# Kernel tuning notes

Measured on AMD Instinct MI355X. Metric: run time of the kernel, lower is better.

## Reference

```python
import jax, jax.numpy as jnp
import numpy as np


def setup_inputs() -> dict:
    key = jax.random.key(0)
    ks = jax.random.split(key, 8)
    B, C, H, W = 16, 256, 64, 64
    E, heads, R = 256, 8, 64
    s = 0.02  # small init scale in lieu of xavier
    return {
        "x": jax.random.normal(ks[0], (B, C, H, W), dtype=jnp.float32),
        "Wqkv": jax.random.normal(ks[1], (3 * E, C), dtype=jnp.float32) * s,
        "bqkv": jnp.zeros((3 * E,), dtype=jnp.float32),
        "Wr": jax.random.normal(ks[2], (2 * R * heads, C), dtype=jnp.float32) * s,
        "br": jnp.zeros((2 * R * heads,), dtype=jnp.float32),
        "Wout": jax.random.normal(ks[3], (C, E), dtype=jnp.float32) * s,
        "bout": jnp.zeros((C,), dtype=jnp.float32),
        "alpha": jax.random.normal(ks[4], (1,), dtype=jnp.float32),
        "num_heads": heads,
        "num_regions": R,
    }


def reference(x, Wqkv, bqkv, Wr, br, Wout, bout, alpha, num_heads, num_regions):
    B, C, H, W = x.shape
    N = H * W
    E = Wqkv.shape[0] // 3
    d = E // num_heads  # head_dim
    xf = x.reshape(B, C, N)  # [B, C, N]

    # qkv 1x1 conv -> [B, 3E, N] -> [B, h, N, 3d] -> q,k,v [B, h, N, d]
    qkv = jnp.einsum("oc,bcn->bon", Wqkv, xf) + bqkv[:, None]
    qkv = qkv.reshape(B, num_heads, 3 * d, N).transpose(0, 1, 3, 2)
    q, k, v = jnp.split(qkv, 3, axis=-1)

    # region projections: 1x1 conv + softmax over the FULL channel axis (2*R*heads)
    r = jnp.einsum("oc,bcn->bon", Wr, xf) + br[:, None]
    r = jax.nn.softmax(r, axis=1)
    r = r.reshape(B, num_heads, 2 * num_regions, N).transpose(0, 1, 3, 2)
    Rq, Rk = jnp.split(r, 2, axis=-1)  # each [B, h, N, R]

    # pool tokens into regions: [B, h, d, R]
    qr = jnp.einsum("bhnd,bhnr->bhdr", q, Rq)
    kr = jnp.einsum("bhnd,bhnr->bhdr", k, Rk)
    vr = jnp.einsum("bhnd,bhnr->bhdr", v, Rk)

    # region-level attention [B, h, Rq, Rk], scaled by sqrt(head_dim)
    logits = jnp.einsum("bhdq,bhdk->bhqk", qr, kr) / jnp.sqrt(jnp.asarray(d, x.dtype))
    attn = jax.nn.softmax(logits, axis=-1)  # dropout is identity at eval

    # values = v_r @ attn^T -> [B, h, d, Rq]; expand back to tokens via Rq^T
    vals = jnp.einsum("bhdk,bhqk->bhdq", vr, attn)
    vals = jnp.einsum("bhdq,bhnq->bhdn", vals, Rq)  # [B, h, d, N]

    vals = vals.reshape(B, E, N)
    out = jnp.einsum("oe,ben->bon", Wout, vals) + bout[:, None]
    out = out.reshape(B, C, H, W)
    return x + alpha * out
```

## Files before the change

kernel.cpp:

```cpp
#include <hip/hip_runtime.h>
#include <cstdint>

typedef unsigned short ushort_t;
typedef __attribute__((ext_vector_type(4))) unsigned short ushort4_t;
typedef __attribute__((ext_vector_type(8))) unsigned short ushort8_t;
typedef __attribute__((ext_vector_type(8))) __bf16 bf16x8;
typedef __attribute__((ext_vector_type(4))) float f32x4;

constexpr int NB = 16;
constexpr int NC = 256;
constexpr int NN = 4096;
constexpr int NP = 1024;
constexpr int NT = 512;
constexpr int NO = 768;

static __device__ __forceinline__ ushort_t f2b(float f) {
  uint32_t u = __builtin_bit_cast(uint32_t, f);
  u += 0x7FFFu + ((u >> 16) & 1u);
  return (ushort_t)(u >> 16);
}
static __device__ __forceinline__ float b2f(ushort_t h) {
  return __builtin_bit_cast(float, (uint32_t)h << 16);
}
static __device__ __forceinline__ f32x4 mfma16(bf16x8 a, bf16x8 b, f32x4 c) {
  return __builtin_amdgcn_mfma_f32_16x16x32_bf16(a, b, c, 0, 0, 0);
}
typedef __attribute__((address_space(1))) const unsigned int guint;
typedef __attribute__((address_space(3))) unsigned int luint;
static __device__ __forceinline__ void glds16(const void* g, void* l) {
  __builtin_amdgcn_global_load_lds((guint*)g, (luint*)l, 16, 0, 0);
}

template <int KITERS>
__device__ __forceinline__ void gemm_core(const ushort_t* __restrict__ Asrc, size_t lda,
                                          const ushort_t* __restrict__ Bsrc, size_t ldb,
                                          ushort_t* SH, f32x4 (&acc)[4][4], int tid) {
  const int l = tid & 63, w = tid >> 6;
  const int fr = l & 15, kq = (l >> 4) * 8;
  const int rr = l >> 3;
  const int sc = ((l & 7) ^ rr) << 3;
  const int swz = (fr & 7) << 3;
  const int wm = (w >> 1) * 64, wn = (w & 1) * 64;

  auto STAGE = [&](int bi, size_t k0) {
    ushort_t* Ad = SH + bi * 8192;
    ushort_t* Bd = SH + 16384 + bi * 8192;
#pragma unroll
    for (int i = 0; i < 4; i++) {
      const int row = i * 32 + w * 8 + rr;
      glds16(Asrc + (size_t)row * lda + k0 + sc, Ad + (i * 32 + w * 8) * 64);
      glds16(Bsrc + (size_t)row * ldb + k0 + sc, Bd + (i * 32 + w * 8) * 64);
    }
  };

  STAGE(0, 0);
  __syncthreads();
  int cur = 0;
#pragma unroll 1
  for (int it = 0; it < KITERS; it++) {
    if (it + 1 < KITERS) STAGE(cur ^ 1, (size_t)(it + 1) * 64);
    const ushort_t* Ar = SH + cur * 8192;
    const ushort_t* Br = SH + 16384 + cur * 8192;
#pragma unroll
    for (int ks = 0; ks < 2; ks++) {
      const int col = ks * 32 + kq;
      bf16x8 af[4], bf[4];
#pragma unroll
      for (int f = 0; f < 4; f++) {
        af[f] = *(const bf16x8*)&Ar[(wm + f * 16 + fr) * 64 + (col ^ swz)];
        bf[f] = *(const bf16x8*)&Br[(wn + f * 16 + fr) * 64 + (col ^ swz)];
      }
#pragma unroll
      for (int fm = 0; fm < 4; fm++)
#pragma unroll
        for (int fn = 0; fn < 4; fn++)
          acc[fm][fn] = mfma16(af[fm], bf[fn], acc[fm][fn]);
    }
    __syncthreads();
    cur ^= 1;
  }
}

__global__ __launch_bounds__(256) void k0_cvt(const float* __restrict__ x,
                                              ushort_t* __restrict__ xb,
                                              ushort_t* __restrict__ xt) {
  __shared__ ushort_t tr[64][88];
  const int tid = threadIdx.x;
  const int n0 = blockIdx.x * 64, c0 = blockIdx.y * 64, b = blockIdx.z;
  const int cr = (tid >> 4) * 4;
  const int nc4 = (tid & 15) * 4;
#pragma unroll
  for (int i = 0; i < 4; i++) {
    size_t idx = ((size_t)b * NC + c0 + cr + i) * NN + n0 + nc4;
    float4 v = *(const float4*)(x + idx);
    ushort4_t o;
    o[0] = f2b(v.x); o[1] = f2b(v.y); o[2] = f2b(v.z); o[3] = f2b(v.w);
    *(ushort4_t*)(xb + idx) = o;
    tr[nc4 + 0][cr + i] = o[0];
    tr[nc4 + 1][cr + i] = o[1];
    tr[nc4 + 2][cr + i] = o[2];
    tr[nc4 + 3][cr + i] = o[3];
  }
  __syncthreads();
  const int nr = tid >> 2, cc0 = (tid & 3) * 16;
  size_t odx = ((size_t)b * NN + n0 + nr) * NC + c0 + cc0;
  *(ushort8_t*)(xt + odx) = *(const ushort8_t*)&tr[nr][cc0];
  *(ushort8_t*)(xt + odx + 8) = *(const ushort8_t*)&tr[nr][cc0 + 8];
}

__global__ __launch_bounds__(256) void cvt_f2b_k(const float* __restrict__ src,
                                                 ushort_t* __restrict__ dst) {
  int i = (blockIdx.x * 256 + threadIdx.x) * 4;
  float4 v = *(const float4*)(src + i);
  ushort4_t o;
  o[0] = f2b(v.x); o[1] = f2b(v.y); o[2] = f2b(v.z); o[3] = f2b(v.w);
  *(ushort4_t*)(dst + i) = o;
}

__global__ __launch_bounds__(256) void k1_proj(const ushort_t* __restrict__ Wrb,
                                               const ushort_t* __restrict__ xt,
                                               const float* __restrict__ br,
                                               ushort_t* __restrict__ P) {
  __shared__ __align__(16) ushort_t SH[4 * 8192];
  const int tid = threadIdx.x;
  const int ord = blockIdx.x;
  const int L = (ord & 7) * 512 + (ord >> 3);
  const int m0 = (L & 7) * 128;
  const int n0 = ((L >> 3) & 31) * 128;
  const int b = L >> 8;
  const int lane = tid & 63, w = tid >> 6;
  const int wm = (w >> 1) * 64, wn = (w & 1) * 64;
  f32x4 acc[4][4] = {};
  gemm_core<4>(Wrb + (size_t)m0 * NC, NC,
               xt + ((size_t)b * NN + n0) * NC, NC, SH, acc, tid);
  const int col = lane & 15, rb = (lane >> 4) * 4;
#pragma unroll
  for (int fm = 0; fm < 4; fm++)
#pragma unroll
    for (int rg = 0; rg < 4; rg++) {
      int row = wm + fm * 16 + rb + rg;
      float bias = br[m0 + row];
#pragma unroll
      for (int fn = 0; fn < 4; fn++)
        SH[row * 136 + wn + fn * 16 + col] = f2b(acc[fm][fn][rg] + bias);
    }
  __syncthreads();
  const int orow = tid >> 1, half = tid & 1;
  const ushort_t* src = &SH[orow * 136 + half * 64];
  ushort_t* dst = P + ((size_t)b * NP + m0 + orow) * NN + n0 + half * 64;
#pragma unroll
  for (int j = 0; j < 8; j++)
    *(ushort8_t*)(dst + j * 8) = *(const ushort8_t*)(src + j * 8);
}

__global__ __launch_bounds__(512) void k2_softmax(ushort_t* __restrict__ P,
                                                  float* __restrict__ sPpart) {
  __shared__ float red[64][64];
  __shared__ float Mf[64], If[64];
  const int tid = threadIdx.x;
  const int n0 = blockIdx.x * 64, b = blockIdx.y;
  const int cg = tid & 7, pg = tid >> 3;
  ushort_t* base = P + (size_t)b * NP * NN + n0 + cg * 8;

  ushort8_t v[16];
  float m[8];
#pragma unroll
  for (int j = 0; j < 8; j++) m[j] = -3.0e38f;
#pragma unroll
  for (int r = 0; r < 16; r++) {
    v[r] = *(const ushort8_t*)(base + (size_t)(pg * 16 + r) * NN);
#pragma unroll
    for (int j = 0; j < 8; j++) m[j] = fmaxf(m[j], b2f(v[r][j]));
  }
#pragma unroll
  for (int j = 0; j < 8; j++) red[pg][cg * 8 + j] = m[j];
  __syncthreads();
  if (tid < 64) {
    float M = -3.0e38f;
    for (int g = 0; g < 64; g++) M = fmaxf(M, red[g][tid]);
    Mf[tid] = M;
  }
  __syncthreads();
  float mj[8], s[8];
#pragma unroll
  for (int j = 0; j < 8; j++) { mj[j] = Mf[cg * 8 + j]; s[j] = 0.f; }
#pragma unroll
  for (int r = 0; r < 16; r++)
#pragma unroll
    for (int j = 0; j < 8; j++) s[j] += __expf(b2f(v[r][j]) - mj[j]);
#pragma unroll
  for (int j = 0; j < 8; j++) red[pg][cg * 8 + j] = s[j];
  __syncthreads();
  if (tid < 64) {
    float S = 0.f;
    for (int g = 0; g < 64; g++) S += red[g][tid];
    If[tid] = 1.f / S;
  }
  __syncthreads();
  float ij[8];
#pragma unroll
  for (int j = 0; j < 8; j++) ij[j] = If[cg * 8 + j];
#pragma unroll
  for (int r = 0; r < 16; r++) {
    int p = pg * 16 + r;
    ushort8_t o;
    float rs = 0.f;
#pragma unroll
    for (int j = 0; j < 8; j++) {
      float e = __expf(b2f(v[r][j]) - mj[j]) * ij[j];
      o[j] = f2b(e);
      rs += e;
    }
    *(ushort8_t*)(base + (size_t)p * NN) = o;
    rs += __shfl_xor(rs, 1, 64);
    rs += __shfl_xor(rs, 2, 64);
    rs += __shfl_xor(rs, 4, 64);
    if (cg == 0) sPpart[((size_t)blockIdx.x * NB + b) * NP + p] = rs;
  }
}

__global__ __launch_bounds__(256) void k2r_reduce(const float* __restrict__ sPpart,
                                                  float* __restrict__ sP) {
  int idx = blockIdx.x * 256 + threadIdx.x;
  float s = 0.f;
#pragma unroll 8
  for (int bx = 0; bx < 64; bx++) s += sPpart[(size_t)bx * (NB * NP) + idx];
  sP[idx] = s;
}

__global__ __launch_bounds__(256) void k3_pool(const ushort_t* __restrict__ xb,
                                               const ushort_t* __restrict__ P,
                                               float* __restrict__ XR4) {
  __shared__ __align__(16) ushort_t SH[4 * 8192];
  const int tid = threadIdx.x;
  const int ord = blockIdx.x;
  const int L = (ord & 7) * 64 + (ord >> 3);
  const int m0 = (L & 1) * 128;
  const int n0 = ((L >> 1) & 7) * 128;
  const int zz = L >> 4;
  const int b = zz >> 1, ks = zz & 1;
  const int lane = tid & 63, w = tid >> 6;
  const int wm = (w >> 1) * 64, wn = (w & 1) * 64;
  f32x4 acc[4][4] = {};
  const size_t kbeg = (size_t)ks * 2048;
  gemm_core<32>(xb + ((size_t)b * NC + m0) * NN + kbeg, NN,
                P + ((size_t)b * NP + n0) * NN + kbeg, NN, SH, acc, tid);
  const int col = lane & 15, rb = (lane >> 4) * 4;
  float* outp = XR4 + (size_t)(ks * NB + b) * NC * NP;
#pragma unroll
  for (int fm = 0; fm < 4; fm++)
#pragma unroll
    for (int fn = 0; fn < 4; fn++)
#pragma unroll
      for (int rg = 0; rg < 4; rg++) {
        int row = m0 + wm + fm * 16 + rb + rg;
        int cc = n0 + wn + fn * 16 + col;
        outp[(size_t)row * NP + cc] = acc[fm][fn][rg];
      }
}

__global__ __launch_bounds__(256) void k3r_tr(const float* __restrict__ XR4,
                                              ushort_t* __restrict__ XRbT) {
  __shared__ ushort_t tr[64][72];
  const int tid = threadIdx.x;
  const int p0 = blockIdx.x * 64, c0 = blockIdx.y * 64, b = blockIdx.z;
  const size_t slice = (size_t)NB * NC * NP;
  const int row = tid >> 4, col4 = (tid & 15) * 4;
#pragma unroll
  for (int i = 0; i < 4; i++) {
    int c = row + i * 16;
    size_t idx = ((size_t)b * NC + c0 + c) * NP + p0 + col4;
    float4 v0 = *(const float4*)(XR4 + idx);
    float4 v1 = *(const float4*)(XR4 + idx + slice);
    tr[col4 + 0][c] = f2b(v0.x + v1.x);
    tr[col4 + 1][c] = f2b(v0.y + v1.y);
    tr[col4 + 2][c] = f2b(v0.z + v1.z);
    tr[col4 + 3][c] = f2b(v0.w + v1.w);
  }
  __syncthreads();
  const int prow = tid >> 2, coff = (tid & 3) * 16;
  size_t odx = ((size_t)b * NP + p0 + prow) * NC + c0 + coff;
  *(ushort8_t*)(XRbT + odx) = *(const ushort8_t*)&tr[prow][coff];
  *(ushort8_t*)(XRbT + odx + 8) = *(const ushort8_t*)&tr[prow][coff + 8];
}

__global__ __launch_bounds__(256) void k4a_qkvr(const ushort_t* __restrict__ Wqkvb,
                                                const ushort_t* __restrict__ XRbT,
                                                const float* __restrict__ bqkv,
                                                const float* __restrict__ sP,
                                                ushort_t* __restrict__ QKVRb) {
  __shared__ __align__(16) ushort_t SH[4 * 8192];
  const int tid = threadIdx.x;
  const int ord = blockIdx.x;
  const int L = (ord & 7) * 96 + (ord >> 3);
  const int m0 = (L % 6) * 128;
  const int rest = L / 6;
  const int n0 = (rest & 7) * 128;
  const int b = rest >> 3;
  const int lane = tid & 63, w = tid >> 6;
  const int wm = (w >> 1) * 64, wn = (w & 1) * 64;
  f32x4 acc[4][4] = {};
  gemm_core<4>(Wqkvb + (size_t)m0 * NC, NC,
               XRbT + ((size_t)b * NP + n0) * NC, NC, SH, acc, tid);
  const int col = lane & 15, rb = (lane >> 4) * 4;
  float spv[4];
#pragma unroll
  for (int fn = 0; fn < 4; fn++) spv[fn] = sP[(size_t)b * NP + n0 + wn + fn * 16 + col];
#pragma unroll
  for (int fm = 0; fm < 4; fm++)
#pragma unroll
    for (int rg = 0; rg < 4; rg++) {
      int row = m0 + wm + fm * 16 + rb + rg;
      float bq = bqkv[row];
#pragma unroll
      for (int fn = 0; fn < 4; fn++) {
        int cc = n0 + wn + fn * 16 + col;
        QKVRb[((size_t)b * NO + row) * NP + cc] = f2b(acc[fm][fn][rg] + bq * spv[fn]);
      }
    }
}

__global__ __launch_bounds__(256) void k4b_attn(const ushort_t* __restrict__ QKVRb,
                                                const float* __restrict__ Wout,
                                                ushort_t* __restrict__ Tmb) {
  const int b = blockIdx.x >> 3, h = blockIdx.x & 7;
  const int tid = threadIdx.x;
  __shared__ float qf[96][64];
  __shared__ float attn_sT[64][65];
  __shared__ float vals_s[32][64];
#pragma unroll
  for (int i = 0; i < 3; i++) {
    int u = i * 256 + tid;
    int rw = u >> 3, jc = (u & 7) * 8;
    int p0 = h * 128 + ((rw < 32) ? 0 : 64);
    ushort8_t v = *(const ushort8_t*)(QKVRb + ((size_t)b * NO + h * 96 + rw) * NP + p0 + jc);
#pragma unroll
    for (int j = 0; j < 8; j++) qf[rw][jc + j] = b2f(v[j]);
  }
  __syncthreads();
  const int lj = tid & 63;
  const int rq = tid >> 6;
  float kcol[32];
#pragma unroll
  for (int dd = 0; dd < 32; dd++) kcol[dd] = qf[32 + dd][lj];
  const float isc = 0.17677669529663687f;
#pragma unroll
  for (int r = 0; r < 16; r++) {
    int qi = r * 4 + rq;
    float a = 0.f;
#pragma unroll
    for (int dd = 0; dd < 32; dd++) a += qf[dd][qi] * kcol[dd];
    attn_sT[lj][qi] = a * isc;
  }
  __syncthreads();
  if (tid < 64) {
    float m = -3e38f;
    for (int k = 0; k < 64; k++) m = fmaxf(m, attn_sT[k][tid]);
    float s = 0.f;
    for (int k = 0; k < 64; k++) {
      float e = __expf(attn_sT[k][tid] - m);
      attn_sT[k][tid] = e;
      s += e;
    }
    float inv = 1.f / s;
    for (int k = 0; k < 64; k++) attn_sT[k][tid] *= inv;
  }
  __syncthreads();
  float acol[64];
#pragma unroll
  for (int k = 0; k < 64; k++) acol[k] = attn_sT[k][lj];
#pragma unroll
  for (int r = 0; r < 8; r++) {
    int dd = r * 4 + rq;
    float a = 0.f;
#pragma unroll
    for (int k = 0; k < 64; k++) a += qf[64 + dd][k] * acol[k];
    vals_s[dd][lj] = a;
  }
  __syncthreads();
  float vcol[32];
#pragma unroll
  for (int dd = 0; dd < 32; dd++) vcol[dd] = vals_s[dd][lj];
  for (int r = 0; r < 64; r++) {
    int c = r * 4 + rq;
    const float4* wp = (const float4*)(Wout + (size_t)c * NC + h * 32);
    float a = 0.f;
#pragma unroll
    for (int t = 0; t < 8; t++) {
      float4 w = wp[t];
      a += w.x * vcol[t * 4] + w.y * vcol[t * 4 + 1] + w.z * vcol[t * 4 + 2] +
           w.w * vcol[t * 4 + 3];
    }
    Tmb[((size_t)b * NC + c) * NT + h * 64 + lj] = f2b(a);
  }
}

__global__ __launch_bounds__(256) void k5_out(const float* __restrict__ x,
                                              const ushort_t* __restrict__ P,
                                              const ushort_t* __restrict__ Tmb,
                                              const float* __restrict__ bout,
                                              const float* __restrict__ alpha,
                                              float* __restrict__ out) {
  __shared__ __align__(16) ushort_t Ash[2 * 8192];
  __shared__ __align__(16) ushort_t Bsh[2 * 9216];
  const int tid = threadIdx.x;
  const int ord = blockIdx.x;
  const int L = (ord & 7) * 128 + (ord >> 3);
  const int m0 = (L & 1) * 128;
  const int n0 = ((L >> 1) & 31) * 128;
  const int b = L >> 6;
  const int lane = tid & 63, w = tid >> 6;
  const int wm = (w >> 1) * 64, wn = (w & 1) * 64;
  const int fr = lane & 15, kq = (lane >> 4) * 8;
  const int rr = lane >> 3, sc = ((lane & 7) ^ rr) << 3;
  const int swz = (fr & 7) << 3;
  const ushort_t* Asrc = Tmb + ((size_t)b * NC + m0) * NT;
  const int kg = tid >> 5, ng = (tid & 31) * 4;
  f32x4 acc[4][4] = {};
  ushort4_t bv[8];

  auto A_STAGE = [&](int bi, int k0) {
    ushort_t* Ad = Ash + bi * 8192;
#pragma unroll
    for (int i = 0; i < 4; i++) {
      const int row = i * 32 + w * 8 + rr;
      glds16(Asrc + (size_t)row * NT + k0 + sc, Ad + (i * 32 + w * 8) * 64);
    }
  };
  auto B_LOAD = [&](int k0) {
#pragma unroll
    for (int i = 0; i < 8; i++) {
      int hj = k0 + kg * 8 + i;
      int prow = ((hj >> 6) << 7) + (hj & 63);
      bv[i] = *(const ushort4_t*)(P + ((size_t)b * NP + prow) * NN + n0 + ng);
    }
  };
  auto B_WRITE = [&](int bi) {
#pragma unroll
    for (int jj = 0; jj < 4; jj++) {
      ushort8_t pk;
#pragma unroll
      for (int i = 0; i < 8; i++) pk[i] = bv[i][jj];
      *(ushort8_t*)&Bsh[bi * 9216 + (ng + jj) * 72 + kg * 8] = pk;
    }
  };

  A_STAGE(0, 0);
  B_LOAD(0);
  B_WRITE(0);
  __syncthreads();
  int cur = 0;
#pragma unroll 1
  for (int it = 0; it < 8; it++) {
    if (it + 1 < 8) {
      A_STAGE(cur ^ 1, (it + 1) * 64);
      B_LOAD((it + 1) * 64);
    }
    const ushort_t* Ar = Ash + cur * 8192;
    const ushort_t* Br = Bsh + cur * 9216;
#pragma unroll
    for (int ks = 0; ks < 2; ks++) {
      const int col = ks * 32 + kq;
      bf16x8 af[4], bf[4];
#pragma unroll
      for (int f = 0; f < 4; f++) {
        af[f] = *(const bf16x8*)&Ar[(wm + f * 16 + fr) * 64 + (col ^ swz)];
        bf[f] = *(const bf16x8*)&Br[(wn + f * 16 + fr) * 72 + col];
      }
#pragma unroll
      for (int fm = 0; fm < 4; fm++)
#pragma unroll
        for (int fn = 0; fn < 4; fn++)
          acc[fm][fn] = mfma16(af[fm], bf[fn], acc[fm][fn]);
    }
    if (it + 1 < 8) B_WRITE(cur ^ 1);
    __syncthreads();
    cur ^= 1;
  }
  const float al = alpha[0];
  const int col = lane & 15, rb = (lane >> 4) * 4;
#pragma unroll
  for (int fm = 0; fm < 4; fm++)
#pragma unroll
    for (int rg = 0; rg < 4; rg++) {
      int row = m0 + wm + fm * 16 + rb + rg;
      float bias = bout[row];
#pragma unroll
      for (int fn = 0; fn < 4; fn++) {
        int cc = n0 + wn + fn * 16 + col;
        size_t idx = ((size_t)b * NC + row) * NN + cc;
        out[idx] = x[idx] + al * (acc[fm][fn][rg] + bias);
      }
    }
}

extern "C" void kernel_launch(void* const* d_in, const int* in_sizes, int n_in,
                              void* d_out, int out_size, void* d_ws, size_t ws_size,
                              hipStream_t stream) {
  const float* x = (const float*)d_in[0];
  const float* Wqkv = (const float*)d_in[1];
  const float* bqkv = (const float*)d_in[2];
  const float* Wr = (const float*)d_in[3];
  const float* br = (const float*)d_in[4];
  const float* Wout = (const float*)d_in[5];
  const float* bout = (const float*)d_in[6];
  const float* alpha = (const float*)d_in[7];
  float* out = (float*)d_out;

  char* ws = (char*)d_ws;
  ushort_t* P = (ushort_t*)ws;
  ushort_t* xb = (ushort_t*)(ws + 134217728);
  ushort_t* XRbT = (ushort_t*)(ws + 134217728);
  ushort_t* xt = (ushort_t*)(ws + 167772160);
  float* XR4 = (float*)(ws + 167772160);
  ushort_t* QKVRb = (ushort_t*)(ws + 167772160);
  ushort_t* Wrb = (ushort_t*)(ws + 201326592);
  float* sPpart = (float*)(ws + 201850880);
  ushort_t* Wqkvb = (ushort_t*)(ws + 201850880);
  float* sP = (float*)(ws + 206045184);
  ushort_t* Tmb = (ushort_t*)(ws + 206110720);

  k0_cvt<<<dim3(64, 4, 16), 256, 0, stream>>>(x, xb, xt);
  cvt_f2b_k<<<256, 256, 0, stream>>>(Wr, Wrb);
  k1_proj<<<4096, 256, 0, stream>>>(Wrb, xt, br, P);
  k2_softmax<<<dim3(64, 16), 512, 0, stream>>>(P, sPpart);
  k2r_reduce<<<64, 256, 0, stream>>>(sPpart, sP);
  cvt_f2b_k<<<192, 256, 0, stream>>>(Wqkv, Wqkvb);
  k3_pool<<<512, 256, 0, stream>>>(xb, P, XR4);
  k3r_tr<<<dim3(16, 4, 16), 256, 0, stream>>>(XR4, XRbT);
  k4a_qkvr<<<768, 256, 0, stream>>>(Wqkvb, XRbT, bqkv, sP, QKVRb);
  k4b_attn<<<128, 256, 0, stream>>>(QKVRb, Wout, Tmb);
  k5_out<<<1024, 256, 0, stream>>>(x, P, Tmb, bout, alpha, out);
}
```

Measured before the change: 328.1 us.

## Enlarge projection GEMM tiles, drop split-K in pooling, fuse transpose epilogue

The region-projection GEMM moves to 256x256 tiles with 512 threads, so each block reuses more of each staged operand and fewer blocks are launched. The pooling GEMM no longer splits K in two. It writes bf16 transposed output directly through shared memory, which removes the fp32 partial buffer and the separate transpose/reduce kernel. The qkv GEMM uses a single-buffered core with half the LDS. Risks: pooling now launches only 256 blocks, which may underfill the GPU. The larger k1 tiles raise register pressure (32 accumulators per lane), and k1 loses its double buffering.

```diff
diff --git a/kernel.cpp b/kernel.cpp
--- a/kernel.cpp
+++ b/kernel.cpp
@@ -32,43 +32,35 @@
 }
 
 template <int KITERS>
-__device__ __forceinline__ void gemm_core(const ushort_t* __restrict__ Asrc, size_t lda,
-                                          const ushort_t* __restrict__ Bsrc, size_t ldb,
-                                          ushort_t* SH, f32x4 (&acc)[4][4], int tid) {
+__device__ __forceinline__ void gemm_core_sb(const ushort_t* __restrict__ Asrc, size_t lda,
+                                             const ushort_t* __restrict__ Bsrc, size_t ldb,
+                                             ushort_t* SH, f32x4 (&acc)[4][4], int tid) {
   const int l = tid & 63, w = tid >> 6;
   const int fr = l & 15, kq = (l >> 4) * 8;
   const int rr = l >> 3;
   const int sc = ((l & 7) ^ rr) << 3;
   const int swz = (fr & 7) << 3;
   const int wm = (w >> 1) * 64, wn = (w & 1) * 64;
-
-  auto STAGE = [&](int bi, size_t k0) {
-    ushort_t* Ad = SH + bi * 8192;
-    ushort_t* Bd = SH + 16384 + bi * 8192;
+  ushort_t* As = SH;
+  ushort_t* Bs = SH + 8192;
+#pragma unroll 1
+  for (int it = 0; it < KITERS; it++) {
+    const size_t k0 = (size_t)it * 64;
 #pragma unroll
     for (int i = 0; i < 4; i++) {
       const int row = i * 32 + w * 8 + rr;
-      glds16(Asrc + (size_t)row * lda + k0 + sc, Ad + (i * 32 + w * 8) * 64);
-      glds16(Bsrc + (size_t)row * ldb + k0 + sc, Bd + (i * 32 + w * 8) * 64);
-    }
-  };
-
-  STAGE(0, 0);
-  __syncthreads();
-  int cur = 0;
-#pragma unroll 1
-  for (int it = 0; it < KITERS; it++) {
-    if (it + 1 < KITERS) STAGE(cur ^ 1, (size_t)(it + 1) * 64);
-    const ushort_t* Ar = SH + cur * 8192;
-    const ushort_t* Br = SH + 16384 + cur * 8192;
+      glds16(Asrc + (size_t)row * lda + k0 + sc, As + (i * 32 + w * 8) * 64);
+      glds16(Bsrc + (size_t)row * ldb + k0 + sc, Bs + (i * 32 + w * 8) * 64);
+    }
+    __syncthreads();
 #pragma unroll
     for (int ks = 0; ks < 2; ks++) {
       const int col = ks * 32 + kq;
       bf16x8 af[4], bf[4];
 #pragma unroll
       for (int f = 0; f < 4; f++) {
-        af[f] = *(const bf16x8*)&Ar[(wm + f * 16 + fr) * 64 + (col ^ swz)];
-        bf[f] = *(const bf16x8*)&Br[(wn + f * 16 + fr) * 64 + (col ^ swz)];
+        af[f] = *(const bf16x8*)&As[(wm + f * 16 + fr) * 64 + (col ^ swz)];
+        bf[f] = *(const bf16x8*)&Bs[(wn + f * 16 + fr) * 64 + (col ^ swz)];
       }
 #pragma unroll
       for (int fm = 0; fm < 4; fm++)
@@ -77,7 +69,6 @@
           acc[fm][fn] = mfma16(af[fm], bf[fn], acc[fm][fn]);
     }
     __syncthreads();
-    cur ^= 1;
   }
 }
 
@@ -117,40 +108,80 @@
   *(ushort4_t*)(dst + i) = o;
 }
 
-__global__ __launch_bounds__(256) void k1_proj(const ushort_t* __restrict__ Wrb,
+__global__ __launch_bounds__(512) void k1_proj(const ushort_t* __restrict__ Wrb,
                                                const ushort_t* __restrict__ xt,
                                                const float* __restrict__ br,
                                                ushort_t* __restrict__ P) {
-  __shared__ __align__(16) ushort_t SH[4 * 8192];
+  __shared__ __align__(16) ushort_t SH[32768];
   const int tid = threadIdx.x;
   const int ord = blockIdx.x;
-  const int L = (ord & 7) * 512 + (ord >> 3);
-  const int m0 = (L & 7) * 128;
-  const int n0 = ((L >> 3) & 31) * 128;
-  const int b = L >> 8;
-  const int lane = tid & 63, w = tid >> 6;
-  const int wm = (w >> 1) * 64, wn = (w & 1) * 64;
-  f32x4 acc[4][4] = {};
-  gemm_core<4>(Wrb + (size_t)m0 * NC, NC,
-               xt + ((size_t)b * NN + n0) * NC, NC, SH, acc, tid);
-  const int col = lane & 15, rb = (lane >> 4) * 4;
-#pragma unroll
-  for (int fm = 0; fm < 4; fm++)
-#pragma unroll
-    for (int rg = 0; rg < 4; rg++) {
-      int row = wm + fm * 16 + rb + rg;
-      float bias = br[m0 + row];
-#pragma unroll
-      for (int fn = 0; fn < 4; fn++)
-        SH[row * 136 + wn + fn * 16 + col] = f2b(acc[fm][fn][rg] + bias);
-    }
-  __syncthreads();
-  const int orow = tid >> 1, half = tid & 1;
-  const ushort_t* src = &SH[orow * 136 + half * 64];
-  ushort_t* dst = P + ((size_t)b * NP + m0 + orow) * NN + n0 + half * 64;
-#pragma unroll
-  for (int j = 0; j < 8; j++)
-    *(ushort8_t*)(dst + j * 8) = *(const ushort8_t*)(src + j * 8);
+  const int L = (ord & 7) * 128 + (ord >> 3);
+  const int m0 = (L & 3) * 256;
+  const int n0 = ((L >> 2) & 15) * 256;
+  const int b = L >> 6;
+  const int l = tid & 63, w = tid >> 6;
+  const int wr = w >> 2, wc = w & 3;
+  const int fr = l & 15, kq = (l >> 4) * 8;
+  const int swz = (fr & 7) << 3;
+  ushort_t* As = SH;
+  ushort_t* Bs = SH + 16384;
+  const ushort_t* Asrc = Wrb + (size_t)m0 * NC;
+  const ushort_t* Bsrc = xt + ((size_t)b * NN + n0) * NC;
+  f32x4 acc[8][4] = {};
+#pragma unroll 1
+  for (int k0 = 0; k0 < NC; k0 += 64) {
+#pragma unroll
+    for (int rnd = 0; rnd < 4; rnd++) {
+      const int rbase = rnd * 64 + w * 8;
+      const int row = rbase + (l >> 3);
+      const int sc = ((l & 7) ^ (row & 7)) << 3;
+      glds16(Asrc + (size_t)row * NC + k0 + sc, As + rbase * 64);
+      glds16(Bsrc + (size_t)row * NC + k0 + sc, Bs + rbase * 64);
+    }
+    __syncthreads();
+#pragma unroll
+    for (int ks = 0; ks < 2; ks++) {
+      const int col = ks * 32 + kq;
+      bf16x8 af[8], bf[4];
+#pragma unroll
+      for (int f = 0; f < 8; f++)
+        af[f] = *(const bf16x8*)&As[(wr * 128 + f * 16 + fr) * 64 + (col ^ swz)];
+#pragma unroll
+      for (int f = 0; f < 4; f++)
+        bf[f] = *(const bf16x8*)&Bs[(wc * 64 + f * 16 + fr) * 64 + (col ^ swz)];
+#pragma unroll
+      for (int fm = 0; fm < 8; fm++)
+#pragma unroll
+        for (int fn = 0; fn < 4; fn++)
+          acc[fm][fn] = mfma16(af[fm], bf[fn], acc[fm][fn]);
+    }
+    __syncthreads();
+  }
+  const int colc = l & 15, rb = (l >> 4) * 4;
+#pragma unroll 1
+  for (int pp = 0; pp < 4; pp++) {
+    if ((w >> 2) == (pp >> 1)) {
+      const int fmb = (pp & 1) * 4;
+#pragma unroll
+      for (int fm = 0; fm < 4; fm++)
+#pragma unroll
+        for (int rg = 0; rg < 4; rg++) {
+          const int rl = fm * 16 + rb + rg;
+          const float bias = br[m0 + pp * 64 + rl];
+#pragma unroll
+          for (int fn = 0; fn < 4; fn++)
+            SH[rl * 264 + wc * 64 + fn * 16 + colc] = f2b(acc[fmb + fm][fn][rg] + bias);
+        }
+    }
+    __syncthreads();
+    const int orow = tid >> 3, c8 = (tid & 7) * 32;
+    ushort_t* dst = P + ((size_t)b * NP + m0 + pp * 64 + orow) * NN + n0 + c8;
+    const ushort_t* s = &SH[orow * 264 + c8];
+#pragma unroll
+    for (int j = 0; j < 4; j++)
+      *(ushort8_t*)(dst + j * 8) = *(const ushort8_t*)(s + j * 8);
+    __syncthreads();
+  }
 }
 
 __global__ __launch_bounds__(512) void k2_softmax(ushort_t* __restrict__ P,
@@ -230,58 +261,86 @@
 
 __global__ __launch_bounds__(256) void k3_pool(const ushort_t* __restrict__ xb,
                                                const ushort_t* __restrict__ P,
-                                               float* __restrict__ XR4) {
+                                               ushort_t* __restrict__ XRbT) {
   __shared__ __align__(16) ushort_t SH[4 * 8192];
   const int tid = threadIdx.x;
   const int ord = blockIdx.x;
-  const int L = (ord & 7) * 64 + (ord >> 3);
+  const int L = (ord & 7) * 32 + (ord >> 3);
   const int m0 = (L & 1) * 128;
   const int n0 = ((L >> 1) & 7) * 128;
-  const int zz = L >> 4;
-  const int b = zz >> 1, ks = zz & 1;
-  const int lane = tid & 63, w = tid >> 6;
+  const int b = L >> 4;
+  const int l = tid & 63, w = tid >> 6;
+  const int fr = l & 15, kq = (l >> 4) * 8;
+  const int rr = l >> 3;
+  const int sc = ((l & 7) ^ rr) << 3;
+  const int swz = (fr & 7) << 3;
   const int wm = (w >> 1) * 64, wn = (w & 1) * 64;
+  const ushort_t* Asrc = xb + ((size_t)b * NC + m0) * NN;
+  const ushort_t* Bsrc = P + ((size_t)b * NP + n0) * NN;
   f32x4 acc[4][4] = {};
-  const size_t kbeg = (size_t)ks * 2048;
-  gemm_core<32>(xb + ((size_t)b * NC + m0) * NN + kbeg, NN,
-                P + ((size_t)b * NP + n0) * NN + kbeg, NN, SH, acc, tid);
-  const int col = lane & 15, rb = (lane >> 4) * 4;
-  float* outp = XR4 + (size_t)(ks * NB + b) * NC * NP;
-#pragma unroll
-  for (int fm = 0; fm < 4; fm++)
-#pragma unroll
-    for (int fn = 0; fn < 4; fn++)
-#pragma unroll
-      for (int rg = 0; rg < 4; rg++) {
-        int row = m0 + wm + fm * 16 + rb + rg;
-        int cc = n0 + wn + fn * 16 + col;
-        outp[(size_t)row * NP + cc] = acc[fm][fn][rg];
+
+  auto STAGE = [&](int bi, size_t k0) {
+    ushort_t* Ad = SH + bi * 8192;
+    ushort_t* Bd = SH + 16384 + bi * 8192;
+#pragma unroll
+    for (int i = 0; i < 4; i++) {
+      const int row = i * 32 + w * 8 + rr;
+      glds16(Asrc + (size_t)row * NN + k0 + sc, Ad + (i * 32 + w * 8) * 64);
+      glds16(Bsrc + (size_t)row * NN + k0 + sc, Bd + (i * 32 + w * 8) * 64);
+    }
+  };
+
+  STAGE(0, 0);
+  __syncthreads();
+  int cur = 0;
+#pragma unroll 1
+  for (int it = 0; it < 64; it++) {
+    if (it + 1 < 64) STAGE(cur ^ 1, (size_t)(it + 1) * 64);
+    const ushort_t* Ar = SH + cur * 8192;
+    const ushort_t* Br = SH + 16384 + cur * 8192;
+#pragma unroll
+    for (int ks = 0; ks < 2; ks++) {
+      const int col = ks * 32 + kq;
+      bf16x8 af[4], bf[4];
+#pragma unroll
+      for (int f = 0; f < 4; f++) {
+        af[f] = *(const bf16x8*)&Ar[(wm + f * 16 + fr) * 64 + (col ^ swz)];
+        bf[f] = *(const bf16x8*)&Br[(wn + f * 16 + fr) * 64 + (col ^ swz)];
       }
-}
-
-__global__ __launch_bounds__(256) void k3r_tr(const float* __restrict__ XR4,
-                                              ushort_t* __restrict__ XRbT) {
-  __shared__ ushort_t tr[64][72];
-  const int tid = threadIdx.x;
-  const int p0 = blockIdx.x * 64, c0 = blockIdx.y * 64, b = blockIdx.z;
-  const size_t slice = (size_t)NB * NC * NP;
-  const int row = tid >> 4, col4 = (tid & 15) * 4;
-#pragma unroll
-  for (int i = 0; i < 4; i++) {
-    int c = row + i * 16;
-    size_t idx = ((size_t)b * NC + c0 + c) * NP + p0 + col4;
-    float4 v0 = *(const float4*)(XR4 + idx);
-    float4 v1 = *(const float4*)(XR4 + idx + slice);
-    tr[col4 + 0][c] = f2b(v0.x + v1.x);
-    tr[col4 + 1][c] = f2b(v0.y + v1.y);
-    tr[col4 + 2][c] = f2b(v0.z + v1.z);
-    tr[col4 + 3][c] = f2b(v0.w + v1.w);
-  }
-  __syncthreads();
-  const int prow = tid >> 2, coff = (tid & 3) * 16;
-  size_t odx = ((size_t)b * NP + p0 + prow) * NC + c0 + coff;
-  *(ushort8_t*)(XRbT + odx) = *(const ushort8_t*)&tr[prow][coff];
-  *(ushort8_t*)(XRbT + odx + 8) = *(const ushort8_t*)&tr[prow][coff + 8];
+#pragma unroll
+      for (int fm = 0; fm < 4; fm++)
+#pragma unroll
+        for (int fn = 0; fn < 4; fn++)
+          acc[fm][fn] = mfma16(af[fm], bf[fn], acc[fm][fn]);
+    }
+    __syncthreads();
+    cur ^= 1;
+  }
+  const int colc = l & 15, rb = (l >> 4) * 4;
+#pragma unroll 1
+  for (int pp = 0; pp < 2; pp++) {
+    if ((w & 1) == pp) {
+#pragma unroll
+      for (int fm = 0; fm < 4; fm++)
+#pragma unroll
+        for (int rg = 0; rg < 4; rg++) {
+          const int cl = wm + fm * 16 + rb + rg;
+#pragma unroll
+          for (int fn = 0; fn < 4; fn++) {
+            const int pl = fn * 16 + colc;
+            SH[pl * 136 + cl] = f2b(acc[fm][fn][rg]);
+          }
+        }
+    }
+    __syncthreads();
+    const int prow = tid >> 2, cch = (tid & 3) * 32;
+    ushort_t* dst = XRbT + ((size_t)b * NP + n0 + pp * 64 + prow) * NC + m0 + cch;
+    const ushort_t* s = &SH[prow * 136 + cch];
+#pragma unroll
+    for (int j = 0; j < 4; j++)
+      *(ushort8_t*)(dst + j * 8) = *(const ushort8_t*)(s + j * 8);
+    __syncthreads();
+  }
 }
 
 __global__ __launch_bounds__(256) void k4a_qkvr(const ushort_t* __restrict__ Wqkvb,
@@ -289,7 +348,7 @@
                                                 const float* __restrict__ bqkv,
                                                 const float* __restrict__ sP,
                                                 ushort_t* __restrict__ QKVRb) {
-  __shared__ __align__(16) ushort_t SH[4 * 8192];
+  __shared__ __align__(16) ushort_t SH[2 * 8192];
   const int tid = threadIdx.x;
   const int ord = blockIdx.x;
   const int L = (ord & 7) * 96 + (ord >> 3);
@@ -300,8 +359,8 @@
   const int lane = tid & 63, w = tid >> 6;
   const int wm = (w >> 1) * 64, wn = (w & 1) * 64;
   f32x4 acc[4][4] = {};
-  gemm_core<4>(Wqkvb + (size_t)m0 * NC, NC,
-               XRbT + ((size_t)b * NP + n0) * NC, NC, SH, acc, tid);
+  gemm_core_sb<4>(Wqkvb + (size_t)m0 * NC, NC,
+                  XRbT + ((size_t)b * NP + n0) * NC, NC, SH, acc, tid);
   const int col = lane & 15, rb = (lane >> 4) * 4;
   float spv[4];
 #pragma unroll
@@ -510,10 +569,9 @@
   char* ws = (char*)d_ws;
   ushort_t* P = (ushort_t*)ws;
   ushort_t* xb = (ushort_t*)(ws + 134217728);
-  ushort_t* XRbT = (ushort_t*)(ws + 134217728);
+  ushort_t* QKVRb = (ushort_t*)(ws + 134217728);
   ushort_t* xt = (ushort_t*)(ws + 167772160);
-  float* XR4 = (float*)(ws + 167772160);
-  ushort_t* QKVRb = (ushort_t*)(ws + 167772160);
+  ushort_t* XRbT = (ushort_t*)(ws + 167772160);
   ushort_t* Wrb = (ushort_t*)(ws + 201326592);
   float* sPpart = (float*)(ws + 201850880);
   ushort_t* Wqkvb = (ushort_t*)(ws + 201850880);
@@ -522,12 +580,11 @@
 
   k0_cvt<<<dim3(64, 4, 16), 256, 0, stream>>>(x, xb, xt);
   cvt_f2b_k<<<256, 256, 0, stream>>>(Wr, Wrb);
-  k1_proj<<<4096, 256, 0, stream>>>(Wrb, xt, br, P);
+  k1_proj<<<1024, 512, 0, stream>>>(Wrb, xt, br, P);
   k2_softmax<<<dim3(64, 16), 512, 0, stream>>>(P, sPpart);
   k2r_reduce<<<64, 256, 0, stream>>>(sPpart, sP);
   cvt_f2b_k<<<192, 256, 0, stream>>>(Wqkv, Wqkvb);
-  k3_pool<<<512, 256, 0, stream>>>(xb, P, XR4);
-  k3r_tr<<<dim3(16, 4, 16), 256, 0, stream>>>(XR4, XRbT);
+  k3_pool<<<256, 256, 0, stream>>>(xb, P, XRbT);
   k4a_qkvr<<<768, 256, 0, stream>>>(Wqkvb, XRbT, bqkv, sP, QKVRb);
   k4b_attn<<<128, 256, 0, stream>>>(QKVRb, Wout, Tmb);
   k5_out<<<1024, 256, 0, stream>>>(x, P, Tmb, bout, alpha, out);
```

New measurement: 1.013 ms. 209% more time.
